# Optimization experiments

Measured on AMD Instinct MI355X. Metric: run time of the kernel, lower is better.

## Reference

```python
import jax, jax.numpy as jnp
import numpy as np

# SigKernel config (from init_kwargs)
SCALES = np.array([1.0], dtype=np.float32)
S0, S1 = 0.0, 1.0   # s0, S
T0, T1 = 0.0, 1.0   # t0, T
REFINEMENT = 1.0    # refinement_factor (new grid == old grid => interp is identity)


def _interpolate(X, t_min, t_max, refinement_factor):
    """Linear interpolation of batched paths (B, L, D) onto a refined uniform grid."""
    L = X.shape[1]
    new_L = int(refinement_factor * (L - 1)) + 1
    t = jnp.linspace(t_min, t_max, L)
    t_new = jnp.linspace(t_min, t_max, new_L)
    interp_ch = lambda ch: jnp.interp(t_new, t, ch)            # (L,) -> (new_L,)
    interp_path = lambda p: jax.vmap(interp_ch, in_axes=1, out_axes=1)(p)
    return jax.vmap(interp_path)(X)


def _solve_pde_single(inc):
    """Second-order finite-difference Goursat solve of K_st = inc * K.

    inc: (m, m) increment matrix. Returns K[m, m] (scalar), with boundary K[i,0]=K[0,j]=1.
    Wavefront recursion over the 2m-1 interior antidiagonals via lax.scan; each
    diagonal is stored as a length-(m+1) vector indexed by the row i (col j = d - i).
    """
    m = inc.shape[0]
    n = m + 1
    idx = jnp.arange(n)
    K0 = jnp.where(idx == 0, 1.0, 0.0)   # antidiagonal d=0
    K1 = jnp.where(idx <= 1, 1.0, 0.0)   # antidiagonal d=1

    def step(carry, d):
        Km2, Km1 = carry                 # diagonals d-2, d-1
        j = d - idx
        ir = jnp.clip(idx - 1, 0, m - 1)
        jc = jnp.clip(j - 1, 0, m - 1)
        a = inc[ir, jc]                  # inc[i-1, j-1] along the diagonal
        f1 = 1.0 + 0.5 * a + (a * a) * (1.0 / 12.0)
        f2 = 1.0 - (a * a) * (1.0 / 12.0)
        # K[i,j] = (K[i,j-1] + K[i-1,j]) * f1 - K[i-1,j-1] * f2
        Kij = (Km1 + jnp.roll(Km1, 1)) * f1 - jnp.roll(Km2, 1) * f2
        Kd = jnp.where((idx == 0) | (j == 0), 1.0, Kij)      # boundary = 1
        Kd = jnp.where((j >= 0) & (j <= m), Kd, 0.0)         # off-diagonal mask
        return (Km1, Kd), None

    (_, Klast), _ = jax.lax.scan(step, (K0, K1), jnp.arange(2, 2 * m + 1))
    return Klast[m]  # K at (m, m)


def _sig_kernel_matrix(X, Y, scale):
    # linear static kernel k(x,y) = scale^2 <x,y>  =>  grid increments of k
    dX = X[:, 1:, :] - X[:, :-1, :]   # (bx, m, d)
    dY = Y[:, 1:, :] - Y[:, :-1, :]   # (by, m, d)
    inc = (scale * scale) * jnp.einsum('aic,bjc->abij', dX, dY)  # (bx, by, m, m)
    return jax.vmap(jax.vmap(_solve_pde_single))(inc)            # (bx, by)


def reference(X, Y):
    Xi = _interpolate(X, S0, S1, REFINEMENT)
    Yi = _interpolate(Y, T0, T1, REFINEMENT)
    scales = jnp.asarray(SCALES)
    ks = jax.vmap(lambda s: _sig_kernel_matrix(Xi, Yi, s))(scales)
    return jnp.mean(ks, axis=0)


def setup_inputs() -> dict:
    key = jax.random.key(0)
    kx, ky = jax.random.split(key)
    bx, by, L, d = 32, 32, 256, 8
    # 0.05 scaling keeps the (exponentially growing) PDE solution well-conditioned
    X = 0.05 * jax.random.normal(kx, (bx, L, d), dtype=jnp.float32)
    Y = 0.05 * jax.random.normal(ky, (by, L, d), dtype=jnp.float32)
    return {"X": X, "Y": Y}
```

## Files before the change

### kernel.cpp

```cpp
#include <hip/hip_runtime.h>


typedef float f32x2 __attribute__((ext_vector_type(2)));
typedef float f32x4 __attribute__((ext_vector_type(4)));

#define MM   255
#define DYST 9
#define DYSZ 3456

static __device__ inline f32x2 fma2(f32x2 a, f32x2 b, f32x2 c) {
    return __builtin_elementwise_fma(a, b, c);
}

__global__ __launch_bounds__(64) void sigker_strip3(
    const float* __restrict__ X,
    const float* __restrict__ Y,
    float* __restrict__ out)
{
    const int pair = blockIdx.x;
    const int ax = pair >> 5;
    const int by = pair & 31;
    const int l  = threadIdx.x;

    __shared__ float dYs[DYSZ];

    const float* Xa = X + ax * 2048;
    const float* Yb = Y + by * 2048;

    #pragma unroll 6
    for (int v = l; v < DYSZ; v += 64) dYs[v] = 0.0f;
    __syncthreads();
    for (int v = l; v < MM * 8; v += 64) {
        const int j = v >> 3, c = v & 7;
        dYs[(j + 63) * DYST + c] = Yb[(j + 1) * 8 + c] - Yb[j * 8 + c];
    }

    f32x4 f[10];
    const f32x4* Xv = (const f32x4*)(Xa + l * 32);
    #pragma unroll
    for (int k = 0; k < 8; ++k) f[k] = Xv[k];
    f[8] = (l < 63) ? Xv[8] : (f32x4)0.0f;
    f[9] = (l < 63) ? Xv[9] : (f32x4)0.0f;

    f32x2 dxp0[8], dxp1[8];
    #pragma unroll
    for (int c = 0; c < 8; ++c) {
        const float e0 = f[(c)      >> 2][(c)      & 3];
        const float e1 = f[(8 + c)  >> 2][(8 + c)  & 3];
        const float e2 = f[(16 + c) >> 2][(16 + c) & 3];
        const float e3 = f[(24 + c) >> 2][(24 + c) & 3];
        const float e4 = f[(32 + c) >> 2][(32 + c) & 3];
        dxp0[c] = (f32x2){e1 - e0, e2 - e1};
        dxp1[c] = (f32x2){e3 - e2, e4 - e3};
    }

    __syncthreads();

    const f32x2 C12  = { 1.0f / 12.0f,  1.0f / 12.0f};
    const f32x2 CN12 = {-1.0f / 12.0f, -1.0f / 12.0f};
    const f32x2 CH   = { 0.5f, 0.5f};
    const f32x2 C1   = { 1.0f, 1.0f};

    float K0 = 1.0f, K1 = 1.0f, K2 = 1.0f, K3 = 1.0f, upd = 1.0f;

    int base = (63 - l) * DYST;
    float dy0 = dYs[base + 0], dy1 = dYs[base + 1];
    float dy2 = dYs[base + 2], dy3 = dYs[base + 3];
    float dy4 = dYs[base + 4], dy5 = dYs[base + 5];
    float dy6 = dYs[base + 6], dy7 = dYs[base + 7];

    #pragma unroll 2
    for (int s = 1; s <= MM + 63; ++s) {
        const int nb = base + DYST;
        const float ny0 = dYs[nb + 0], ny1 = dYs[nb + 1];
        const float ny2 = dYs[nb + 2], ny3 = dYs[nb + 3];
        const float ny4 = dYs[nb + 4], ny5 = dYs[nb + 5];
        const float ny6 = dYs[nb + 6], ny7 = dYs[nb + 7];

        float up = __shfl_up(K3, 1);
        if (l == 0) up = 1.0f;

        f32x2 b;
        b = (f32x2){dy0, dy0};
        f32x2 a01 = dxp0[0] * b, a23 = dxp1[0] * b;
        b = (f32x2){dy1, dy1};
        a01 = fma2(dxp0[1], b, a01); a23 = fma2(dxp1[1], b, a23);
        b = (f32x2){dy2, dy2};
        a01 = fma2(dxp0[2], b, a01); a23 = fma2(dxp1[2], b, a23);
        b = (f32x2){dy3, dy3};
        a01 = fma2(dxp0[3], b, a01); a23 = fma2(dxp1[3], b, a23);
        b = (f32x2){dy4, dy4};
        a01 = fma2(dxp0[4], b, a01); a23 = fma2(dxp1[4], b, a23);
        b = (f32x2){dy5, dy5};
        a01 = fma2(dxp0[5], b, a01); a23 = fma2(dxp1[5], b, a23);
        b = (f32x2){dy6, dy6};
        a01 = fma2(dxp0[6], b, a01); a23 = fma2(dxp1[6], b, a23);
        b = (f32x2){dy7, dy7};
        a01 = fma2(dxp0[7], b, a01); a23 = fma2(dxp1[7], b, a23);

        const f32x2 q01 = a01 * a01, q23 = a23 * a23;
        const f32x2 f1a = fma2(q01, C12, fma2(a01, CH, C1));
        const f32x2 f1b = fma2(q23, C12, fma2(a23, CH, C1));
        const f32x2 f2a = fma2(q01, CN12, C1);
        const f32x2 f2b = fma2(q23, CN12, C1);

        const float t0 = upd * f2a.x;
        const float k0 = fmaf(K0 + up, f1a.x, -t0);
        const float t1 = K0 * f2a.y;
        const float k1 = fmaf(K1 + k0, f1a.y, -t1);
        const float t2 = K1 * f2b.x;
        const float k2 = fmaf(K2 + k1, f1b.x, -t2);
        const float t3 = K2 * f2b.y;
        const float k3 = fmaf(K3 + k2, f1b.y, -t3);

        upd = up; K0 = k0; K1 = k1; K2 = k2; K3 = k3;
        dy0 = ny0; dy1 = ny1; dy2 = ny2; dy3 = ny3;
        dy4 = ny4; dy5 = ny5; dy6 = ny6; dy7 = ny7;
        base = nb;
    }

    if (l == 63) out[pair] = K2;
}

extern "C" void kernel_launch(void* const* d_in, const int* in_sizes, int n_in,
                              void* d_out, int out_size, void* d_ws, size_t ws_size,
                              hipStream_t stream)
{
    const float* X = (const float*)d_in[0];
    const float* Y = (const float*)d_in[1];
    float* out = (float*)d_out;
    (void)in_sizes; (void)n_in; (void)out_size; (void)d_ws; (void)ws_size;

    sigker_strip3<<<dim3(32 * 32), dim3(64), 0, stream>>>(X, Y, out);
}
```

Before: 46.17 us.

## Use DPP row shift for neighbor exchange and software-pipeline factor computation

Swaps the __shfl_up cross-lane exchange for a DPP update with control 0x138, with the value 1.0 as the old operand, so lane 0 gets 1 without a branch. Moves the computation of the increment factors one step ahead and prefetches dY two rows ahead, taking the factor math and LDS latency off the serial wavefront chain. Regroups the recurrence so the K-independent terms are computed before the dependent FMA chain, shortening the critical path. Also vectorizes the shared-memory zeroing. Risk: DPP 0x138 (wave_shr:1 per public ISA docs) may not shift across 16-lane rows as shfl_up does, which could make results wrong.

```diff
diff --git a/kernel.cpp b/kernel.cpp
--- a/kernel.cpp
+++ b/kernel.cpp
@@ -12,7 +12,14 @@
     return __builtin_elementwise_fma(a, b, c);
 }
 
-__global__ __launch_bounds__(64) void sigker_strip3(
+static __device__ inline float shr1_or_one(float x) {
+    int r = __builtin_amdgcn_update_dpp(
+        __float_as_int(1.0f), __float_as_int(x),
+        0x138 , 0xF, 0xF, false);
+    return __int_as_float(r);
+}
+
+__global__ __launch_bounds__(64) void sigker_dpp(
     const float* __restrict__ X,
     const float* __restrict__ Y,
     float* __restrict__ out)
@@ -27,33 +34,36 @@
     const float* Xa = X + ax * 2048;
     const float* Yb = Y + by * 2048;
 
-    #pragma unroll 6
-    for (int v = l; v < DYSZ; v += 64) dYs[v] = 0.0f;
+    {
+        f32x4* dz = (f32x4*)dYs;
+        #pragma unroll
+        for (int v = l; v < DYSZ / 4; v += 64) dz[v] = (f32x4){0, 0, 0, 0};
+    }
     __syncthreads();
     for (int v = l; v < MM * 8; v += 64) {
         const int j = v >> 3, c = v & 7;
         dYs[(j + 63) * DYST + c] = Yb[(j + 1) * 8 + c] - Yb[j * 8 + c];
     }
 
-    f32x4 f[10];
-    const f32x4* Xv = (const f32x4*)(Xa + l * 32);
-    #pragma unroll
-    for (int k = 0; k < 8; ++k) f[k] = Xv[k];
-    f[8] = (l < 63) ? Xv[8] : (f32x4)0.0f;
-    f[9] = (l < 63) ? Xv[9] : (f32x4)0.0f;
-
     f32x2 dxp0[8], dxp1[8];
-    #pragma unroll
-    for (int c = 0; c < 8; ++c) {
-        const float e0 = f[(c)      >> 2][(c)      & 3];
-        const float e1 = f[(8 + c)  >> 2][(8 + c)  & 3];
-        const float e2 = f[(16 + c) >> 2][(16 + c) & 3];
-        const float e3 = f[(24 + c) >> 2][(24 + c) & 3];
-        const float e4 = f[(32 + c) >> 2][(32 + c) & 3];
-        dxp0[c] = (f32x2){e1 - e0, e2 - e1};
-        dxp1[c] = (f32x2){e3 - e2, e4 - e3};
+    {
+        f32x4 f[10];
+        const f32x4* Xv = (const f32x4*)(Xa + l * 32);
+        #pragma unroll
+        for (int k = 0; k < 8; ++k) f[k] = Xv[k];
+        f[8] = (l < 63) ? Xv[8] : (f32x4){0, 0, 0, 0};
+        f[9] = (l < 63) ? Xv[9] : (f32x4){0, 0, 0, 0};
+        #pragma unroll
+        for (int c = 0; c < 8; ++c) {
+            const float e0 = f[(c)      >> 2][(c)      & 3];
+            const float e1 = f[(8 + c)  >> 2][(8 + c)  & 3];
+            const float e2 = f[(16 + c) >> 2][(16 + c) & 3];
+            const float e3 = f[(24 + c) >> 2][(24 + c) & 3];
+            const float e4 = f[(32 + c) >> 2][(32 + c) & 3];
+            dxp0[c] = (f32x2){e1 - e0, e2 - e1};
+            dxp1[c] = (f32x2){e3 - e2, e4 - e3};
+        }
     }
-
     __syncthreads();
 
     const f32x2 C12  = { 1.0f / 12.0f,  1.0f / 12.0f};
@@ -61,62 +71,67 @@
     const f32x2 CH   = { 0.5f, 0.5f};
     const f32x2 C1   = { 1.0f, 1.0f};
 
+    auto factors = [&](const float* dy, f32x2& f1a, f32x2& f1b,
+                       f32x2& f2a, f32x2& f2b) {
+        f32x2 b = (f32x2){dy[0], dy[0]};
+        f32x2 a01 = dxp0[0] * b, a23 = dxp1[0] * b;
+        #pragma unroll
+        for (int c = 1; c < 8; ++c) {
+            b = (f32x2){dy[c], dy[c]};
+            a01 = fma2(dxp0[c], b, a01);
+            a23 = fma2(dxp1[c], b, a23);
+        }
+        const f32x2 q01 = a01 * a01, q23 = a23 * a23;
+        f1a = fma2(q01, C12, fma2(a01, CH, C1));
+        f1b = fma2(q23, C12, fma2(a23, CH, C1));
+        f2a = fma2(q01, CN12, C1);
+        f2b = fma2(q23, CN12, C1);
+    };
+
     float K0 = 1.0f, K1 = 1.0f, K2 = 1.0f, K3 = 1.0f, upd = 1.0f;
 
-    int base = (63 - l) * DYST;
-    float dy0 = dYs[base + 0], dy1 = dYs[base + 1];
-    float dy2 = dYs[base + 2], dy3 = dYs[base + 3];
-    float dy4 = dYs[base + 4], dy5 = dYs[base + 5];
-    float dy6 = dYs[base + 6], dy7 = dYs[base + 7];
+    const int base = (63 - l) * DYST;
+    float dyN[8];
+    f32x2 f1a, f1b, f2a, f2b;
+    {
+        float dyA[8];
+        #pragma unroll
+        for (int c = 0; c < 8; ++c) dyA[c] = dYs[base + c];
+        factors(dyA, f1a, f1b, f2a, f2b);
+        #pragma unroll
+        for (int c = 0; c < 8; ++c) dyN[c] = dYs[base + DYST + c];
+    }
+    int pbase = base + 2 * DYST;
 
     #pragma unroll 2
     for (int s = 1; s <= MM + 63; ++s) {
-        const int nb = base + DYST;
-        const float ny0 = dYs[nb + 0], ny1 = dYs[nb + 1];
-        const float ny2 = dYs[nb + 2], ny3 = dYs[nb + 3];
-        const float ny4 = dYs[nb + 4], ny5 = dYs[nb + 5];
-        const float ny6 = dYs[nb + 6], ny7 = dYs[nb + 7];
+        float dyP[8];
+        #pragma unroll
+        for (int c = 0; c < 8; ++c) dyP[c] = dYs[pbase + c];
 
-        float up = __shfl_up(K3, 1);
-        if (l == 0) up = 1.0f;
-
-        f32x2 b;
-        b = (f32x2){dy0, dy0};
-        f32x2 a01 = dxp0[0] * b, a23 = dxp1[0] * b;
-        b = (f32x2){dy1, dy1};
-        a01 = fma2(dxp0[1], b, a01); a23 = fma2(dxp1[1], b, a23);
-        b = (f32x2){dy2, dy2};
-        a01 = fma2(dxp0[2], b, a01); a23 = fma2(dxp1[2], b, a23);
-        b = (f32x2){dy3, dy3};
-        a01 = fma2(dxp0[3], b, a01); a23 = fma2(dxp1[3], b, a23);
-        b = (f32x2){dy4, dy4};
-        a01 = fma2(dxp0[4], b, a01); a23 = fma2(dxp1[4], b, a23);
-        b = (f32x2){dy5, dy5};
-        a01 = fma2(dxp0[5], b, a01); a23 = fma2(dxp1[5], b, a23);
-        b = (f32x2){dy6, dy6};
-        a01 = fma2(dxp0[6], b, a01); a23 = fma2(dxp1[6], b, a23);
-        b = (f32x2){dy7, dy7};
-        a01 = fma2(dxp0[7], b, a01); a23 = fma2(dxp1[7], b, a23);
-
-        const f32x2 q01 = a01 * a01, q23 = a23 * a23;
-        const f32x2 f1a = fma2(q01, C12, fma2(a01, CH, C1));
-        const f32x2 f1b = fma2(q23, C12, fma2(a23, CH, C1));
-        const f32x2 f2a = fma2(q01, CN12, C1);
-        const f32x2 f2b = fma2(q23, CN12, C1);
+        const float up = shr1_or_one(K3);
 
         const float t0 = upd * f2a.x;
-        const float k0 = fmaf(K0 + up, f1a.x, -t0);
-        const float t1 = K0 * f2a.y;
-        const float k1 = fmaf(K1 + k0, f1a.y, -t1);
-        const float t2 = K1 * f2b.x;
-        const float k2 = fmaf(K2 + k1, f1b.x, -t2);
-        const float t3 = K2 * f2b.y;
-        const float k3 = fmaf(K3 + k2, f1b.y, -t3);
+        const float t1 = K0  * f2a.y;
+        const float t2 = K1  * f2b.x;
+        const float t3 = K2  * f2b.y;
+        const float c0 = fmaf(K0, f1a.x, -t0);
+        const float c1 = fmaf(K1, f1a.y, -t1);
+        const float c2 = fmaf(K2, f1b.x, -t2);
+        const float c3 = fmaf(K3, f1b.y, -t3);
+
+        const float k0 = fmaf(up, f1a.x, c0);
+        const float k1 = fmaf(k0, f1a.y, c1);
+        const float k2 = fmaf(k1, f1b.x, c2);
+        const float k3 = fmaf(k2, f1b.y, c3);
 
         upd = up; K0 = k0; K1 = k1; K2 = k2; K3 = k3;
-        dy0 = ny0; dy1 = ny1; dy2 = ny2; dy3 = ny3;
-        dy4 = ny4; dy5 = ny5; dy6 = ny6; dy7 = ny7;
-        base = nb;
+
+        factors(dyN, f1a, f1b, f2a, f2b);
+
+        #pragma unroll
+        for (int c = 0; c < 8; ++c) dyN[c] = dyP[c];
+        pbase += DYST;
     }
 
     if (l == 63) out[pair] = K2;
@@ -131,5 +146,5 @@
     float* out = (float*)d_out;
     (void)in_sizes; (void)n_in; (void)out_size; (void)d_ws; (void)ws_size;
 
-    sigker_strip3<<<dim3(32 * 32), dim3(64), 0, stream>>>(X, Y, out);
+    sigker_dpp<<<dim3(32 * 32), dim3(64), 0, stream>>>(X, Y, out);
 }
```

Result: faster. 41.03 us (-11.1%).
